# Optimization experiments

Hardware: AMD Instinct MI355X
Metric: run time of the kernel (lower is better)

## Reference

```python
import jax, jax.numpy as jnp
import numpy as np

NUM_HEADS = 16
NUM_FEATURES = 1024
HEAD_DIM = NUM_FEATURES // NUM_HEADS
MAX_WAVELENGTH = 10000.0
SCALE_FACTOR = 1.0


def apply_rope(x, positions):
    # x: [B, S, H, D], positions: [B, S]
    half = HEAD_DIM // 2
    fraction = 2.0 * jnp.arange(half, dtype=x.dtype) / HEAD_DIM
    timescale = MAX_WAVELENGTH ** fraction                      # [half]
    sinusoid = positions[..., None].astype(x.dtype) / timescale  # [B, S, half]
    sinusoid = sinusoid[..., None, :] / SCALE_FACTOR             # [B, S, 1, half]
    sin, cos = jnp.sin(sinusoid), jnp.cos(sinusoid)
    x1, x2 = jnp.split(x, 2, axis=-1)
    return jnp.concatenate([x1 * cos - x2 * sin, x2 * cos + x1 * sin], axis=-1).astype(x.dtype)


def setup_inputs() -> dict:
    key = jax.random.key(0)
    ks = jax.random.split(key, 9)
    B, S, F = 2, 2048, NUM_FEATURES
    std = 1.0 / np.sqrt(F)
    inp = {
        "x": jax.random.normal(ks[0], (B, S, F), dtype=jnp.float32),
        "positions": jnp.broadcast_to(jnp.arange(S, dtype=jnp.int32), (B, S)),
        "Wq": jax.random.normal(ks[1], (F, F), dtype=jnp.float32) * std,
        "bq": jnp.zeros((F,), dtype=jnp.float32),
        "Wk": jax.random.normal(ks[2], (F, F), dtype=jnp.float32) * std,
        "bk": jnp.zeros((F,), dtype=jnp.float32),
        "Wv": jax.random.normal(ks[3], (F, F), dtype=jnp.float32) * std,
        "bv": jnp.zeros((F,), dtype=jnp.float32),
        "Wo": jax.random.normal(ks[4], (F, F), dtype=jnp.float32) * std,
        "bo": jnp.zeros((F,), dtype=jnp.float32),
    }
    return inp


def reference(x, positions, Wq, bq, Wk, bk, Wv, bv, Wo, bo):
    B, S, F = x.shape
    H, D = NUM_HEADS, HEAD_DIM
    q = (x @ Wq + bq).reshape(B, S, H, D)
    k = (x @ Wk + bk).reshape(B, S, H, D)
    v = (x @ Wv + bv).reshape(B, S, H, D)
    q = apply_rope(q, positions)
    k = apply_rope(k, positions)
    scale = jnp.sqrt(jnp.asarray(D, dtype=x.dtype))
    # scores: [B, H, S, S]
    scores = jnp.einsum("bqhd,bkhd->bhqk", q, k) / scale
    causal = jnp.tril(jnp.ones((S, S), dtype=bool))
    big_neg = jnp.finfo(scores.dtype).min
    scores = jnp.where(causal, scores, big_neg)
    attn = jax.nn.softmax(scores, axis=-1)
    out = jnp.einsum("bhqk,bkhd->bqhd", attn, v).reshape(B, S, F)
    return out @ Wo + bo
```

## Files before the change

kernel.cpp:

```cpp
#include <hip/hip_runtime.h>
#include <hip/hip_bf16.h>

#define S_LEN 2048
#define NF 1024
#define NH 16
#define HD 64
#define NB 2
#define M_TOT 4096

typedef __bf16 bf16x8 __attribute__((ext_vector_type(8)));
typedef float f32x4 __attribute__((ext_vector_type(4)));
typedef unsigned short u16;

__device__ __forceinline__ u16 f2bf(float f) {
  union { float f; unsigned u; } v; v.f = f;
  unsigned r = v.u + 0x7FFFu + ((v.u >> 16) & 1u);
  return (u16)(r >> 16);
}

__device__ __forceinline__ unsigned pk2bf(float a, float b) {
  __hip_bfloat162 t = __float22bfloat162_rn(make_float2(a, b));
  union { __hip_bfloat162 h; unsigned u; } u; u.h = t; return u.u;
}

__device__ __forceinline__ f32x4 mfma16(bf16x8 a, bf16x8 b, f32x4 c) {
  return __builtin_amdgcn_mfma_f32_16x16x32_bf16(a, b, c, 0, 0, 0);
}

__device__ __forceinline__ void gll16(const u16* g, u16* l) {
  __builtin_amdgcn_global_load_lds(
      (const __attribute__((address_space(1))) unsigned int*)g,
      (__attribute__((address_space(3))) unsigned int*)l, 16, 0, 0);
}

__device__ __forceinline__ u16* swz(u16* base, int row, int chunk) {
  return (u16*)((char*)base + row * 128 + ((chunk ^ (row & 7)) * 16));
}
__device__ __forceinline__ const u16* swz(const u16* base, int row, int chunk) {
  return (const u16*)((const char*)base + row * 128 + ((chunk ^ (row & 7)) * 16));
}

__global__ void __launch_bounds__(256) cast_kernel(const float* __restrict__ in,
                                                   u16* __restrict__ out) {
  int i = (blockIdx.x * 256 + threadIdx.x) * 4;
  float4 v = *(const float4*)(in + i);
  ushort4 o;
  o.x = f2bf(v.x); o.y = f2bf(v.y); o.z = f2bf(v.z); o.w = f2bf(v.w);
  *(ushort4*)(out + i) = o;
}

__global__ void __launch_bounds__(256) rope_table_kernel(const int* __restrict__ positions,
                                                         float2* __restrict__ tab) {
  int idx = blockIdx.x * 256 + threadIdx.x;
  int p = idx & 31;
  int bs = idx >> 5;
  float pos = (float)positions[bs];
  float ang = pos / __powf(10000.0f, (float)p * (1.0f / 32.0f));
  float sn, cs;
  sincosf(ang, &sn, &cs);
  tab[idx] = make_float2(sn, cs);
}

__global__ void __launch_bounds__(256) wtrans_kernel(
    const float* __restrict__ W0, const float* __restrict__ W1,
    const float* __restrict__ W2, const float* __restrict__ W3,
    u16* __restrict__ T0, u16* __restrict__ T1,
    u16* __restrict__ T2, u16* __restrict__ T3) {
  const float* W = (blockIdx.z == 0) ? W0 : (blockIdx.z == 1) ? W1 : (blockIdx.z == 2) ? W2 : W3;
  u16* Wt = (blockIdx.z == 0) ? T0 : (blockIdx.z == 1) ? T1 : (blockIdx.z == 2) ? T2 : T3;
  __shared__ float t[32][33];
  int n0 = blockIdx.x * 32, k0 = blockIdx.y * 32;
  int tx = threadIdx.x, ty0 = threadIdx.y;
#pragma unroll
  for (int i = 0; i < 4; i++) {
    int ty = ty0 + i * 8;
    t[ty][tx] = W[(size_t)(k0 + ty) * NF + n0 + tx];
  }
  __syncthreads();
#pragma unroll
  for (int i = 0; i < 4; i++) {
    int ty = ty0 + i * 8;
    Wt[(size_t)(n0 + ty) * NF + k0 + tx] = f2bf(t[tx][ty]);
  }
}

__device__ __forceinline__ void mm_core(const u16* __restrict__ A, const u16* __restrict__ Bt,
                                        int m0, int n0, int kstart,
                                        u16* As, u16* Bs, f32x4 acc[4][4]) {
  const int tid = threadIdx.x;
  const int lane = tid & 63, w = tid >> 6;
  const int l15 = lane & 15, quad = lane >> 4;
  const int wr = w >> 1, wc = w & 1;
#pragma unroll
  for (int i = 0; i < 4; i++)
#pragma unroll
    for (int j = 0; j < 4; j++) {
      f32x4 z = {0.f, 0.f, 0.f, 0.f};
      acc[i][j] = z;
    }
  const u16* gA[4];
  const u16* gB[4];
#pragma unroll
  for (int i = 0; i < 4; i++) {
    int ci = i * 256 + tid;
    int row = ci >> 3, col = (ci & 7) ^ (row & 7);
    gA[i] = &A[(size_t)(m0 + row) * NF + col * 8];
    gB[i] = &Bt[(size_t)(n0 + row) * NF + col * 8];
  }
  for (int s = 0; s < NF / 64; s++) {
    const int k0 = ((s + kstart) & (NF / 64 - 1)) * 64;
    __syncthreads();
#pragma unroll
    for (int i = 0; i < 4; i++) {
      gll16(gA[i] + k0, &As[(i * 256 + w * 64) * 8]);
      gll16(gB[i] + k0, &Bs[(i * 256 + w * 64) * 8]);
    }
    __syncthreads();
#pragma unroll
    for (int kk = 0; kk < 2; kk++) {
      bf16x8 af[4], bfr[4];
#pragma unroll
      for (int i = 0; i < 4; i++)
        af[i] = *(const bf16x8*)swz(As, wr * 64 + i * 16 + l15, kk * 4 + quad);
#pragma unroll
      for (int j = 0; j < 4; j++)
        bfr[j] = *(const bf16x8*)swz(Bs, wc * 64 + j * 16 + l15, kk * 4 + quad);
#pragma unroll
      for (int i = 0; i < 4; i++)
#pragma unroll
        for (int j = 0; j < 4; j++)
          acc[i][j] = mfma16(af[i], bfr[j], acc[i][j]);
    }
  }
}

#define QSCL 0.18033688f

__global__ void __launch_bounds__(256) gemm_qkv_kernel(
    const u16* __restrict__ xb,
    const u16* __restrict__ wtq, const u16* __restrict__ wtk, const u16* __restrict__ wtv,
    const float* __restrict__ bq, const float* __restrict__ bk, const float* __restrict__ bv,
    const float2* __restrict__ rtab,
    u16* __restrict__ qo, u16* __restrict__ ko, u16* __restrict__ vto) {
  __shared__ u16 As[128 * 64], Bs[128 * 64];
  const int bx = blockIdx.x;
  const int xcd = bx & 7, slot = bx >> 3;
  const int z = slot >> 5, intra = slot & 31;
  const int by = (xcd >> 1) * 8 + (intra >> 2);
  const int bxn = (xcd & 1) * 4 + (intra & 3);
  const int kstart = (intra * 3 + z * 5) & 15;
  const u16* Wt = (z == 0) ? wtq : (z == 1) ? wtk : wtv;
  const float* bias = (z == 0) ? bq : (z == 1) ? bk : bv;
  const int m0 = by * 128, n0 = bxn * 128;
  f32x4 acc[4][4];
  mm_core(xb, Wt, m0, n0, kstart, As, Bs, acc);
  const int tid = threadIdx.x;
  const int lane = tid & 63, w = tid >> 6;
  const int l15 = lane & 15, quad = lane >> 4;
  const int wr = w >> 1, wc = w & 1;
  if (z < 2) {
    u16* out = (z == 0) ? qo : ko;
    const float oscl = (z == 0) ? QSCL : 1.0f;
#pragma unroll
    for (int i = 0; i < 4; i++) {
#pragma unroll
      for (int r = 0; r < 4; r++) {
        int gm = m0 + wr * 64 + i * 16 + quad * 4 + r;
        int b = gm >> 11, s = gm & 2047;
#pragma unroll
        for (int j = 0; j < 2; j++) {
          int col1 = n0 + wc * 64 + j * 16 + l15;
          int p = j * 16 + l15;
          float2 sc = rtab[gm * 32 + p];
          float x1 = acc[i][j][r] + bias[col1];
          float x2 = acc[i][j + 2][r] + bias[col1 + 32];
          float o1 = (x1 * sc.y - x2 * sc.x) * oscl;
          float o2 = (x2 * sc.y + x1 * sc.x) * oscl;
          int h = col1 >> 6;
          size_t base = ((size_t)((b * NH + h) * S_LEN + s)) * HD;
          out[base + p] = f2bf(o1);
          out[base + p + 32] = f2bf(o2);
        }
      }
    }
  } else {
#pragma unroll
    for (int i = 0; i < 4; i++) {
      int gm0 = m0 + wr * 64 + i * 16 + quad * 4;
      int b = gm0 >> 11, s0 = gm0 & 2047;
#pragma unroll
      for (int j = 0; j < 4; j++) {
        int col = n0 + wc * 64 + j * 16 + l15;
        int h = col >> 6, d = col & 63;
        float bb = bias[col];
        ushort4 pk;
        pk.x = f2bf(acc[i][j][0] + bb);
        pk.y = f2bf(acc[i][j][1] + bb);
        pk.z = f2bf(acc[i][j][2] + bb);
        pk.w = f2bf(acc[i][j][3] + bb);
        *(ushort4*)&vto[((size_t)((b * NH + h) * HD + d)) * S_LEN + s0] = pk;
      }
    }
  }
}

__global__ void __launch_bounds__(256) gemm_o_kernel(const u16* __restrict__ ab,
                                                     const u16* __restrict__ wto,
                                                     const float* __restrict__ bo,
                                                     float* __restrict__ out) {
  __shared__ u16 As[128 * 64], Bs[128 * 64];
  const int bxr = blockIdx.x;
  const int xcd = bxr & 7, intra = bxr >> 3;
  const int by = (xcd >> 1) * 8 + (intra >> 2);
  const int bxn = (xcd & 1) * 4 + (intra & 3);
  const int kstart = (intra * 3) & 15;
  const int m0 = by * 128, n0 = bxn * 128;
  f32x4 acc[4][4];
  mm_core(ab, wto, m0, n0, kstart, As, Bs, acc);
  const int tid = threadIdx.x;
  const int lane = tid & 63, w = tid >> 6;
  const int l15 = lane & 15, quad = lane >> 4;
  const int wr = w >> 1, wc = w & 1;
#pragma unroll
  for (int i = 0; i < 4; i++) {
#pragma unroll
    for (int j = 0; j < 4; j++) {
      int col = n0 + wc * 64 + j * 16 + l15;
      float bb = bo[col];
#pragma unroll
      for (int r = 0; r < 4; r++) {
        int gm = m0 + wr * 64 + i * 16 + quad * 4 + r;
        out[(size_t)gm * NF + col] = acc[i][j][r] + bb;
      }
    }
  }
}

__global__ void __launch_bounds__(256) attn_kernel(
    const u16* __restrict__ qb, const u16* __restrict__ kb,
    const u16* __restrict__ vtb, u16* __restrict__ ob) {
  __shared__ u16 ks[64 * 64];
  __shared__ u16 vs[64 * 64];
  __shared__ u16 ps[4][16 * 64];
  const int bx = blockIdx.x;
  const int qt = (bx < 512) ? (31 - (bx >> 5)) : ((bx - 512) >> 5);
  const int bh = bx & 31;
  const int tid = threadIdx.x;
  const int lane = tid & 63, w = tid >> 6, l15 = lane & 15, quad = lane >> 4;
  const int bb = bh >> 4, h = bh & 15;
  const size_t kvbase = (size_t)bh * S_LEN;
  const size_t vbase = (size_t)bh * HD;
  const int Q0 = qt * 64;
  const int nit = qt + 1;
  const int r0 = tid >> 3, c0 = tid & 7;
  const int r1 = r0 + 32;

  bf16x8 ones;
#pragma unroll
  for (int i = 0; i < 8; i++) ones[i] = (__bf16)1.0f;

  bf16x8 qf[2];
  {
    const u16* qrow = &qb[(kvbase + Q0 + w * 16 + l15) * HD];
#pragma unroll
    for (int hh = 0; hh < 2; hh++)
      qf[hh] = *(const bf16x8*)&qrow[hh * 32 + quad * 8];
  }

  float mrun = -1e30f;
  f32x4 Oa[4], lacc;
  { f32x4 z = {0.f, 0.f, 0.f, 0.f}; lacc = z;
#pragma unroll
    for (int t = 0; t < 4; t++) Oa[t] = z; }

  *(uint4*)swz(ks, r0, c0) = *(const uint4*)&kb[(kvbase + r0) * HD + c0 * 8];
  *(uint4*)swz(ks, r1, c0) = *(const uint4*)&kb[(kvbase + r1) * HD + c0 * 8];
  *(uint4*)swz(vs, r0, c0) = *(const uint4*)&vtb[(vbase + r0) * S_LEN + c0 * 8];
  *(uint4*)swz(vs, r1, c0) = *(const uint4*)&vtb[(vbase + r1) * S_LEN + c0 * 8];
  __syncthreads();

  for (int it = 0; it < nit; ++it) {
    const int k0 = it * 64;
    const bool pf = (it + 1 < nit);
    uint4 pk0, pk1, pv0, pv1;
    if (pf) {
      int k1 = k0 + 64;
      pk0 = *(const uint4*)&kb[(kvbase + k1 + r0) * HD + c0 * 8];
      pk1 = *(const uint4*)&kb[(kvbase + k1 + r1) * HD + c0 * 8];
      pv0 = *(const uint4*)&vtb[(vbase + r0) * S_LEN + k1 + c0 * 8];
      pv1 = *(const uint4*)&vtb[(vbase + r1) * S_LEN + k1 + c0 * 8];
    }
    f32x4 sf[4];
#pragma unroll
    for (int t = 0; t < 4; t++) {
      bf16x8 ak0 = *(const bf16x8*)swz(ks, t * 16 + l15, quad);
      bf16x8 ak1 = *(const bf16x8*)swz(ks, t * 16 + l15, 4 + quad);
      f32x4 z = {0.f, 0.f, 0.f, 0.f};
      z = mfma16(ak0, qf[0], z);
      z = mfma16(ak1, qf[1], z);
      sf[t] = z;
    }
    if (it == qt) {
      int qg = Q0 + w * 16 + l15;
#pragma unroll
      for (int t = 0; t < 4; t++)
#pragma unroll
        for (int rr = 0; rr < 4; rr++)
          if (k0 + t * 16 + quad * 4 + rr > qg) sf[t][rr] = -1e30f;
    }
    float alph;
    {
      float mx = sf[0][0];
#pragma unroll
      for (int t = 0; t < 4; t++)
#pragma unroll
        for (int rr = 0; rr < 4; rr++) mx = fmaxf(mx, sf[t][rr]);
      mx = fmaxf(mx, __shfl_xor(mx, 16, 64));
      mx = fmaxf(mx, __shfl_xor(mx, 32, 64));
      float mnew = fmaxf(mrun, mx);
      alph = __builtin_amdgcn_exp2f(mrun - mnew);
      mrun = mnew;
#pragma unroll
      for (int t = 0; t < 4; t++)
#pragma unroll
        for (int rr = 0; rr < 4; rr++)
          sf[t][rr] = __builtin_amdgcn_exp2f(sf[t][rr] - mnew);
    }
    if (__any(alph < 1.f)) {
#pragma unroll
      for (int rr = 0; rr < 4; rr++) {
        float ao = __shfl(alph, quad * 4 + rr, 64);
#pragma unroll
        for (int t = 0; t < 4; t++) Oa[t][rr] *= ao;
        lacc[rr] *= ao;
      }
    }
#pragma unroll
    for (int t = 0; t < 4; t++) {
      uint2 pkk;
      pkk.x = pk2bf(sf[t][0], sf[t][1]);
      pkk.y = pk2bf(sf[t][2], sf[t][3]);
      int chnk = 2 * t + (quad >> 1);
      *(uint2*)((char*)ps[w] + l15 * 128 + ((chnk ^ (l15 & 7)) * 16) + (quad & 1) * 8) = pkk;
    }
    __builtin_amdgcn_wave_barrier();
    bf16x8 ap[2];
#pragma unroll
    for (int hh = 0; hh < 2; hh++)
      ap[hh] = *(const bf16x8*)swz(ps[w], l15, hh * 4 + quad);
#pragma unroll
    for (int t = 0; t < 4; t++) {
      bf16x8 bv0 = *(const bf16x8*)swz(vs, t * 16 + l15, quad);
      bf16x8 bv1 = *(const bf16x8*)swz(vs, t * 16 + l15, 4 + quad);
      Oa[t] = mfma16(ap[0], bv0, Oa[t]);
      Oa[t] = mfma16(ap[1], bv1, Oa[t]);
    }
    lacc = mfma16(ap[0], ones, lacc);
    lacc = mfma16(ap[1], ones, lacc);
    if (pf) {
      __syncthreads();
      *(uint4*)swz(ks, r0, c0) = pk0;
      *(uint4*)swz(ks, r1, c0) = pk1;
      *(uint4*)swz(vs, r0, c0) = pv0;
      *(uint4*)swz(vs, r1, c0) = pv1;
      __syncthreads();
    }
  }

#pragma unroll
  for (int rr = 0; rr < 4; rr++) {
    float inv = 1.f / lacc[rr];
    int qg = Q0 + w * 16 + quad * 4 + rr;
    size_t rowb = ((size_t)(bb * S_LEN + qg)) * NF + h * HD;
#pragma unroll
    for (int t = 0; t < 4; t++)
      ob[rowb + t * 16 + l15] = f2bf(Oa[t][rr] * inv);
  }
}

extern "C" void kernel_launch(void* const* d_in, const int* in_sizes, int n_in,
                              void* d_out, int out_size, void* d_ws, size_t ws_size,
                              hipStream_t stream) {
  const float* x  = (const float*)d_in[0];
  const int* pos  = (const int*)d_in[1];
  const float* Wq = (const float*)d_in[2];
  const float* bq = (const float*)d_in[3];
  const float* Wk = (const float*)d_in[4];
  const float* bk = (const float*)d_in[5];
  const float* Wv = (const float*)d_in[6];
  const float* bv = (const float*)d_in[7];
  const float* Wo = (const float*)d_in[8];
  const float* bo = (const float*)d_in[9];
  float* out = (float*)d_out;

  u16* xb  = (u16*)d_ws;
  u16* wtq = xb + (size_t)M_TOT * NF;
  u16* wtk = wtq + (size_t)NF * NF;
  u16* wtv = wtk + (size_t)NF * NF;
  u16* wto = wtv + (size_t)NF * NF;
  u16* qb  = wto + (size_t)NF * NF;
  u16* kb  = qb + (size_t)M_TOT * NF;
  u16* vtb = kb + (size_t)M_TOT * NF;
  float2* rtab = (float2*)(vtb + (size_t)M_TOT * NF);
  u16* attnb = xb;

  cast_kernel<<<dim3(M_TOT * NF / 1024), 256, 0, stream>>>(x, xb);
  rope_table_kernel<<<dim3(NB * S_LEN * 32 / 256), 256, 0, stream>>>(pos, rtab);
  wtrans_kernel<<<dim3(32, 32, 4), dim3(32, 8), 0, stream>>>(Wq, Wk, Wv, Wo,
                                                             wtq, wtk, wtv, wto);
  gemm_qkv_kernel<<<dim3(768), 256, 0, stream>>>(xb, wtq, wtk, wtv, bq, bk, bv,
                                                 rtab, qb, kb, vtb);
  attn_kernel<<<dim3(1024), 256, 0, stream>>>(qb, kb, vtb, attnb);
  gemm_o_kernel<<<dim3(256), 256, 0, stream>>>(attnb, wto, bo, out);
}
```

Baseline: 200.9 us.

## Double attention KV tile to 128 keys and fuse prep kernels into one launch

The attention kernel now stages 128 keys per iteration: a 128-row K tile and V split into two 64-column halves. This halves the number of loop iterations and block-wide barriers per query tile, and s_setprio is raised around the MFMA sections. For even query tiles the last block computes up to 64 extra masked keys, and the kernel uses more LDS and registers, which may lower occupancy. Separately, the cast, rope-table and weight-transpose kernels are merged into one launch with a block-index dispatch to cut launch overhead.

Measured after the change: 253.4 us. +26.2%, slower.

```diff
diff --git a/kernel.cpp b/kernel.cpp
--- a/kernel.cpp
+++ b/kernel.cpp
@@ -40,47 +40,48 @@
   return (const u16*)((const char*)base + row * 128 + ((chunk ^ (row & 7)) * 16));
 }
 
-__global__ void __launch_bounds__(256) cast_kernel(const float* __restrict__ in,
-                                                   u16* __restrict__ out) {
-  int i = (blockIdx.x * 256 + threadIdx.x) * 4;
-  float4 v = *(const float4*)(in + i);
-  ushort4 o;
-  o.x = f2bf(v.x); o.y = f2bf(v.y); o.z = f2bf(v.z); o.w = f2bf(v.w);
-  *(ushort4*)(out + i) = o;
-}
-
-__global__ void __launch_bounds__(256) rope_table_kernel(const int* __restrict__ positions,
-                                                         float2* __restrict__ tab) {
-  int idx = blockIdx.x * 256 + threadIdx.x;
-  int p = idx & 31;
-  int bs = idx >> 5;
-  float pos = (float)positions[bs];
-  float ang = pos / __powf(10000.0f, (float)p * (1.0f / 32.0f));
-  float sn, cs;
-  sincosf(ang, &sn, &cs);
-  tab[idx] = make_float2(sn, cs);
-}
-
-__global__ void __launch_bounds__(256) wtrans_kernel(
+__global__ void __launch_bounds__(256) prep_kernel(
+    const float* __restrict__ x, u16* __restrict__ xb,
+    const int* __restrict__ positions, float2* __restrict__ rtab,
     const float* __restrict__ W0, const float* __restrict__ W1,
     const float* __restrict__ W2, const float* __restrict__ W3,
     u16* __restrict__ T0, u16* __restrict__ T1,
     u16* __restrict__ T2, u16* __restrict__ T3) {
-  const float* W = (blockIdx.z == 0) ? W0 : (blockIdx.z == 1) ? W1 : (blockIdx.z == 2) ? W2 : W3;
-  u16* Wt = (blockIdx.z == 0) ? T0 : (blockIdx.z == 1) ? T1 : (blockIdx.z == 2) ? T2 : T3;
   __shared__ float t[32][33];
-  int n0 = blockIdx.x * 32, k0 = blockIdx.y * 32;
-  int tx = threadIdx.x, ty0 = threadIdx.y;
-#pragma unroll
-  for (int i = 0; i < 4; i++) {
-    int ty = ty0 + i * 8;
-    t[ty][tx] = W[(size_t)(k0 + ty) * NF + n0 + tx];
-  }
-  __syncthreads();
-#pragma unroll
-  for (int i = 0; i < 4; i++) {
-    int ty = ty0 + i * 8;
-    Wt[(size_t)(n0 + ty) * NF + k0 + tx] = f2bf(t[tx][ty]);
+  const int bx = blockIdx.x, tid = threadIdx.x;
+  if (bx < 4096) {
+    int i = (bx * 256 + tid) * 4;
+    float4 v = *(const float4*)(x + i);
+    ushort4 o;
+    o.x = f2bf(v.x); o.y = f2bf(v.y); o.z = f2bf(v.z); o.w = f2bf(v.w);
+    *(ushort4*)(xb + i) = o;
+  } else if (bx < 4608) {
+    int idx = (bx - 4096) * 256 + tid;
+    int p = idx & 31;
+    int bs = idx >> 5;
+    float pos = (float)positions[bs];
+    float ang = pos / __powf(10000.0f, (float)p * (1.0f / 32.0f));
+    float sn, cs;
+    sincosf(ang, &sn, &cs);
+    rtab[idx] = make_float2(sn, cs);
+  } else {
+    int idx = bx - 4608;
+    int z = idx >> 10, rem = idx & 1023;
+    const float* W = (z == 0) ? W0 : (z == 1) ? W1 : (z == 2) ? W2 : W3;
+    u16* Wt = (z == 0) ? T0 : (z == 1) ? T1 : (z == 2) ? T2 : T3;
+    int n0 = (rem & 31) * 32, k0 = (rem >> 5) * 32;
+    int tx = tid & 31, ty0 = tid >> 5;
+#pragma unroll
+    for (int i = 0; i < 4; i++) {
+      int ty = ty0 + i * 8;
+      t[ty][tx] = W[(size_t)(k0 + ty) * NF + n0 + tx];
+    }
+    __syncthreads();
+#pragma unroll
+    for (int i = 0; i < 4; i++) {
+      int ty = ty0 + i * 8;
+      Wt[(size_t)(n0 + ty) * NF + k0 + tx] = f2bf(t[tx][ty]);
+    }
   }
 }
 
@@ -239,8 +240,8 @@
 __global__ void __launch_bounds__(256) attn_kernel(
     const u16* __restrict__ qb, const u16* __restrict__ kb,
     const u16* __restrict__ vtb, u16* __restrict__ ob) {
-  __shared__ u16 ks[64 * 64];
-  __shared__ u16 vs[64 * 64];
+  __shared__ u16 ks[128 * 64];
+  __shared__ u16 vs[2][64 * 64];
   __shared__ u16 ps[4][16 * 64];
   const int bx = blockIdx.x;
   const int qt = (bx < 512) ? (31 - (bx >> 5)) : ((bx - 512) >> 5);
@@ -251,9 +252,7 @@
   const size_t kvbase = (size_t)bh * S_LEN;
   const size_t vbase = (size_t)bh * HD;
   const int Q0 = qt * 64;
-  const int nit = qt + 1;
-  const int r0 = tid >> 3, c0 = tid & 7;
-  const int r1 = r0 + 32;
+  const int nit = (qt >> 1) + 1;
 
   bf16x8 ones;
 #pragma unroll
@@ -273,26 +272,36 @@
 #pragma unroll
     for (int t = 0; t < 4; t++) Oa[t] = z; }
 
-  *(uint4*)swz(ks, r0, c0) = *(const uint4*)&kb[(kvbase + r0) * HD + c0 * 8];
-  *(uint4*)swz(ks, r1, c0) = *(const uint4*)&kb[(kvbase + r1) * HD + c0 * 8];
-  *(uint4*)swz(vs, r0, c0) = *(const uint4*)&vtb[(vbase + r0) * S_LEN + c0 * 8];
-  *(uint4*)swz(vs, r1, c0) = *(const uint4*)&vtb[(vbase + r1) * S_LEN + c0 * 8];
+#pragma unroll
+  for (int i = 0; i < 4; i++) {
+    int ci = i * 256 + tid;
+    int kr = ci >> 3, kc = ci & 7;
+    *(uint4*)swz(ks, kr, kc) = *(const uint4*)&kb[(kvbase + kr) * HD + kc * 8];
+    int vh = ci >> 9, vr = (ci >> 3) & 63, vc = ci & 7;
+    *(uint4*)swz(&vs[vh][0], vr, vc) =
+        *(const uint4*)&vtb[(vbase + vr) * S_LEN + vh * 64 + vc * 8];
+  }
   __syncthreads();
 
   for (int it = 0; it < nit; ++it) {
-    const int k0 = it * 64;
+    const int k0 = it * 128;
     const bool pf = (it + 1 < nit);
-    uint4 pk0, pk1, pv0, pv1;
+    uint4 pk[4], pv[4];
     if (pf) {
-      int k1 = k0 + 64;
-      pk0 = *(const uint4*)&kb[(kvbase + k1 + r0) * HD + c0 * 8];
-      pk1 = *(const uint4*)&kb[(kvbase + k1 + r1) * HD + c0 * 8];
-      pv0 = *(const uint4*)&vtb[(vbase + r0) * S_LEN + k1 + c0 * 8];
-      pv1 = *(const uint4*)&vtb[(vbase + r1) * S_LEN + k1 + c0 * 8];
-    }
-    f32x4 sf[4];
-#pragma unroll
-    for (int t = 0; t < 4; t++) {
+      int k1 = k0 + 128;
+#pragma unroll
+      for (int i = 0; i < 4; i++) {
+        int ci = i * 256 + tid;
+        int kr = ci >> 3, kc = ci & 7;
+        pk[i] = *(const uint4*)&kb[(kvbase + k1 + kr) * HD + kc * 8];
+        int vh = ci >> 9, vr = (ci >> 3) & 63, vc = ci & 7;
+        pv[i] = *(const uint4*)&vtb[(vbase + vr) * S_LEN + k1 + vh * 64 + vc * 8];
+      }
+    }
+    f32x4 sf[8];
+    __builtin_amdgcn_s_setprio(1);
+#pragma unroll
+    for (int t = 0; t < 8; t++) {
       bf16x8 ak0 = *(const bf16x8*)swz(ks, t * 16 + l15, quad);
       bf16x8 ak1 = *(const bf16x8*)swz(ks, t * 16 + l15, 4 + quad);
       f32x4 z = {0.f, 0.f, 0.f, 0.f};
@@ -300,10 +309,11 @@
       z = mfma16(ak1, qf[1], z);
       sf[t] = z;
     }
-    if (it == qt) {
+    __builtin_amdgcn_s_setprio(0);
+    if (it == nit - 1) {
       int qg = Q0 + w * 16 + l15;
 #pragma unroll
-      for (int t = 0; t < 4; t++)
+      for (int t = 0; t < 8; t++)
 #pragma unroll
         for (int rr = 0; rr < 4; rr++)
           if (k0 + t * 16 + quad * 4 + rr > qg) sf[t][rr] = -1e30f;
@@ -312,7 +322,7 @@
     {
       float mx = sf[0][0];
 #pragma unroll
-      for (int t = 0; t < 4; t++)
+      for (int t = 0; t < 8; t++)
 #pragma unroll
         for (int rr = 0; rr < 4; rr++) mx = fmaxf(mx, sf[t][rr]);
       mx = fmaxf(mx, __shfl_xor(mx, 16, 64));
@@ -321,7 +331,7 @@
       alph = __builtin_amdgcn_exp2f(mrun - mnew);
       mrun = mnew;
 #pragma unroll
-      for (int t = 0; t < 4; t++)
+      for (int t = 0; t < 8; t++)
 #pragma unroll
         for (int rr = 0; rr < 4; rr++)
           sf[t][rr] = __builtin_amdgcn_exp2f(sf[t][rr] - mnew);
@@ -336,33 +346,41 @@
       }
     }
 #pragma unroll
-    for (int t = 0; t < 4; t++) {
-      uint2 pkk;
-      pkk.x = pk2bf(sf[t][0], sf[t][1]);
-      pkk.y = pk2bf(sf[t][2], sf[t][3]);
-      int chnk = 2 * t + (quad >> 1);
-      *(uint2*)((char*)ps[w] + l15 * 128 + ((chnk ^ (l15 & 7)) * 16) + (quad & 1) * 8) = pkk;
-    }
-    __builtin_amdgcn_wave_barrier();
-    bf16x8 ap[2];
-#pragma unroll
-    for (int hh = 0; hh < 2; hh++)
-      ap[hh] = *(const bf16x8*)swz(ps[w], l15, hh * 4 + quad);
-#pragma unroll
-    for (int t = 0; t < 4; t++) {
-      bf16x8 bv0 = *(const bf16x8*)swz(vs, t * 16 + l15, quad);
-      bf16x8 bv1 = *(const bf16x8*)swz(vs, t * 16 + l15, 4 + quad);
-      Oa[t] = mfma16(ap[0], bv0, Oa[t]);
-      Oa[t] = mfma16(ap[1], bv1, Oa[t]);
-    }
-    lacc = mfma16(ap[0], ones, lacc);
-    lacc = mfma16(ap[1], ones, lacc);
+    for (int vh = 0; vh < 2; vh++) {
+#pragma unroll
+      for (int t = 0; t < 4; t++) {
+        f32x4 s4 = sf[vh * 4 + t];
+        uint2 pkk;
+        pkk.x = pk2bf(s4[0], s4[1]);
+        pkk.y = pk2bf(s4[2], s4[3]);
+        int chnk = 2 * t + (quad >> 1);
+        *(uint2*)((char*)ps[w] + l15 * 128 + ((chnk ^ (l15 & 7)) * 16) + (quad & 1) * 8) = pkk;
+      }
+      __builtin_amdgcn_wave_barrier();
+      bf16x8 ap[2];
+#pragma unroll
+      for (int hh = 0; hh < 2; hh++)
+        ap[hh] = *(const bf16x8*)swz(ps[w], l15, hh * 4 + quad);
+      __builtin_amdgcn_s_setprio(1);
+#pragma unroll
+      for (int t = 0; t < 4; t++) {
+        bf16x8 bv0 = *(const bf16x8*)swz(&vs[vh][0], t * 16 + l15, quad);
+        bf16x8 bv1 = *(const bf16x8*)swz(&vs[vh][0], t * 16 + l15, 4 + quad);
+        Oa[t] = mfma16(ap[0], bv0, Oa[t]);
+        Oa[t] = mfma16(ap[1], bv1, Oa[t]);
+      }
+      lacc = mfma16(ap[0], ones, lacc);
+      lacc = mfma16(ap[1], ones, lacc);
+      __builtin_amdgcn_s_setprio(0);
+    }
     if (pf) {
       __syncthreads();
-      *(uint4*)swz(ks, r0, c0) = pk0;
-      *(uint4*)swz(ks, r1, c0) = pk1;
-      *(uint4*)swz(vs, r0, c0) = pv0;
-      *(uint4*)swz(vs, r1, c0) = pv1;
+#pragma unroll
+      for (int i = 0; i < 4; i++) {
+        int ci = i * 256 + tid;
+        *(uint4*)swz(ks, ci >> 3, ci & 7) = pk[i];
+        *(uint4*)swz(&vs[ci >> 9][0], (ci >> 3) & 63, ci & 7) = pv[i];
+      }
       __syncthreads();
     }
   }
@@ -404,10 +422,8 @@
   float2* rtab = (float2*)(vtb + (size_t)M_TOT * NF);
   u16* attnb = xb;
 
-  cast_kernel<<<dim3(M_TOT * NF / 1024), 256, 0, stream>>>(x, xb);
-  rope_table_kernel<<<dim3(NB * S_LEN * 32 / 256), 256, 0, stream>>>(pos, rtab);
-  wtrans_kernel<<<dim3(32, 32, 4), dim3(32, 8), 0, stream>>>(Wq, Wk, Wv, Wo,
-                                                             wtq, wtk, wtv, wto);
+  prep_kernel<<<dim3(8704), 256, 0, stream>>>(x, xb, pos, rtab,
+                                              Wq, Wk, Wv, Wo, wtq, wtk, wtv, wto);
   gemm_qkv_kernel<<<dim3(768), 256, 0, stream>>>(xb, wtq, wtk, wtv, bq, bk, bv,
                                                  rtab, qb, kb, vtb);
   attn_kernel<<<dim3(1024), 256, 0, stream>>>(qb, kb, vtb, attnb);
```
